# Optimization experiments

Measured on AMD Instinct MI355X. Metric: run time of the kernel, lower is better.

The kernel has to match this reference:

```python
import jax, jax.numpy as jnp
import numpy as np

B, T, NINP, NHID = 64, 256, 256, 512
NTOK0, NTOK1 = 2048, 512


def _lstm_cell(x, h, c, Wih, bih, Whh, bhh):
    # PyTorch LSTMCell gate order: i, f, g, o
    g = x @ Wih.T + bih + h @ Whh.T + bhh
    i, f, gg, o = jnp.split(g, 4, axis=-1)
    c_new = jax.nn.sigmoid(f) * c + jax.nn.sigmoid(i) * jnp.tanh(gg)
    h_new = jax.nn.sigmoid(o) * jnp.tanh(c_new)
    return h_new, c_new


def setup_inputs() -> dict:
    key = jax.random.key(0)
    ks = jax.random.split(key, 16)
    ir = 0.1  # initrange from init_weights
    d = {
        "input0": jax.random.randint(ks[0], (B, T), 0, NTOK0),
        "input1": jax.random.randint(ks[1], (B, T), 0, NTOK1),
        "h_low0": jnp.zeros((B, NHID), jnp.float32),
        "c_low0": jnp.zeros((B, NHID), jnp.float32),
        "h_high0": jnp.zeros((B, NHID), jnp.float32),
        "c_high0": jnp.zeros((B, NHID), jnp.float32),
        "measure_token_idx": 5,
        "emb0": jax.random.uniform(ks[2], (NTOK0, NINP), jnp.float32, -ir, ir),
        "emb1": jax.random.uniform(ks[3], (NTOK1, NINP), jnp.float32, -ir, ir),
        # low cell: input size = ninp*2 + nhid = 1024
        "Wih_low": jax.random.normal(ks[4], (4 * NHID, 2 * NINP + NHID), jnp.float32) * 0.02,
        "bih_low": jnp.zeros((4 * NHID,), jnp.float32),
        "Whh_low": jax.random.normal(ks[5], (4 * NHID, NHID), jnp.float32) * 0.02,
        "bhh_low": jnp.zeros((4 * NHID,), jnp.float32),
        # high cell: input size = nhid
        "Wih_high": jax.random.normal(ks[6], (4 * NHID, NHID), jnp.float32) * 0.02,
        "bih_high": jnp.zeros((4 * NHID,), jnp.float32),
        "Whh_high": jax.random.normal(ks[7], (4 * NHID, NHID), jnp.float32) * 0.02,
        "bhh_high": jnp.zeros((4 * NHID,), jnp.float32),
        "Wdec0": jax.random.uniform(ks[8], (NTOK0, NHID), jnp.float32, -ir, ir),
        "bdec0": jnp.zeros((NTOK0,), jnp.float32),
        "Wdec1": jax.random.uniform(ks[9], (NTOK1, NHID), jnp.float32, -ir, ir),
        "bdec1": jnp.zeros((NTOK1,), jnp.float32),
    }
    return d


def reference(input0, input1, h_low0, c_low0, h_high0, c_high0, measure_token_idx,
              emb0, emb1, Wih_low, bih_low, Whh_low, bhh_low,
              Wih_high, bih_high, Whh_high, bhh_high,
              Wdec0, bdec0, Wdec1, bdec1):
    # Embedding lookups for both channels, concatenated (dropout = identity in eval)
    embs = jnp.concatenate([emb0[input0], emb1[input1]], axis=-1)  # [B,T,2*ninp]
    xs = jnp.swapaxes(embs, 0, 1)                                   # [T,B,2*ninp]
    mask = (input0 == measure_token_idx).astype(embs.dtype)[..., None]  # [B,T,1]
    ms = jnp.swapaxes(mask, 0, 1)                                   # [T,B,1]

    def step(carry, xm):
        h_l, c_l, h_h, c_h = carry
        x_t, m_t = xm
        inp = jnp.concatenate([x_t, h_h], axis=-1)  # [B, 2*ninp+nhid]
        h_l, c_l = _lstm_cell(inp, h_l, c_l, Wih_low, bih_low, Whh_low, bhh_low)
        h_tmp, c_tmp = _lstm_cell(h_l, h_h, c_h, Wih_high, bih_high, Whh_high, bhh_high)
        h_h = m_t * h_tmp + (1.0 - m_t) * h_h  # gated state update at measure boundaries
        c_h = m_t * c_tmp + (1.0 - m_t) * c_h
        return (h_l, c_l, h_h, c_h), h_l

    (h_l, c_l, h_h, c_h), outs = jax.lax.scan(step, (h_low0, c_low0, h_high0, c_high0), (xs, ms))
    output = jnp.swapaxes(outs, 0, 1)  # [B,T,nhid]
    dec0 = output @ Wdec0.T + bdec0    # [B,T,ntok0]
    dec1 = output @ Wdec1.T + bdec1    # [B,T,ntok1]
    return dec0, dec1, h_l, c_l, h_h, c_h
```

## Files before the change

### kernel.cpp

```cpp
#include <hip/hip_runtime.h>
#include <hip/hip_bf16.h>

#define T_ 256
#define B_ 64
#define NWG 32

typedef __attribute__((ext_vector_type(8))) short bf16x8;
typedef __attribute__((ext_vector_type(4))) float f32x4;
typedef __attribute__((ext_vector_type(4))) unsigned uint4v;
union v128 { uint4v u4; bf16x8 h8; };

__device__ __forceinline__ float bf2f(unsigned short u){
  unsigned int i = ((unsigned int)u) << 16;
  float f; __builtin_memcpy(&f, &i, 4); return f;
}
__device__ __forceinline__ unsigned short f2bf(float f){
  __hip_bfloat16 h = __float2bfloat16(f);
  unsigned short u; __builtin_memcpy(&u, &h, 2); return u;
}
__device__ __forceinline__ float fsigm(float x){ return 1.0f/(1.0f + __expf(-x)); }
__device__ __forceinline__ float ftanh(float x){ return 1.0f - 2.0f/(__expf(2.0f*x) + 1.0f); }

__device__ __forceinline__ void ld16_cc_issue(v128* dst, const unsigned short* p){
  asm volatile("global_load_dwordx4 %0, %1, off sc0 sc1" : "=v"(dst->u4) : "v"(p) : "memory");
}
__device__ __forceinline__ void st8_cc(unsigned short* p, unsigned long long v){
  asm volatile("global_store_dwordx2 %0, %1, off sc0 sc1" :: "v"(p), "v"(v) : "memory");
}
__device__ __forceinline__ unsigned long long ld8_cc(const unsigned short* p){
  unsigned long long v;
  asm volatile("global_load_dwordx2 %0, %1, off sc0 sc1\n\ts_waitcnt vmcnt(0)"
               : "=v"(v) : "v"(p) : "memory");
  return v;
}

__global__ void k_prep(const int* __restrict__ in0, const int* __restrict__ in1,
                       const int* __restrict__ mtok,
                       const float* __restrict__ emb0, const float* __restrict__ emb1,
                       const float* __restrict__ Wih_low, const float* __restrict__ Whh_low_f,
                       const float* __restrict__ Wih_high_f, const float* __restrict__ Whh_high_f,
                       const float* __restrict__ Wdec0_f, const float* __restrict__ Wdec1_f,
                       unsigned short* __restrict__ W0, unsigned short* __restrict__ Wlh,
                       unsigned short* __restrict__ Whhl, unsigned short* __restrict__ Wihh,
                       unsigned short* __restrict__ Whhh, unsigned short* __restrict__ Wd0,
                       unsigned short* __restrict__ Wd1, unsigned short* __restrict__ E,
                       float* __restrict__ mask, unsigned* __restrict__ stepflag,
                       unsigned* __restrict__ bar)
{
  int gid = blockIdx.x*blockDim.x + threadIdx.x;
  int gsz = gridDim.x*blockDim.x;
  for (int i=gid; i<2048*512; i+=gsz){
    int r = i>>9, c = i&511;
    W0[i]   = f2bf(Wih_low[(size_t)r*1024 + c]);
    Wlh[i]  = f2bf(Wih_low[(size_t)r*1024 + 512 + c]);
    Whhl[i] = f2bf(Whh_low_f[i]);
    Wihh[i] = f2bf(Wih_high_f[i]);
    Whhh[i] = f2bf(Whh_high_f[i]);
    Wd0[i]  = f2bf(Wdec0_f[i]);
  }
  for (int i=gid; i<512*512; i+=gsz) Wd1[i] = f2bf(Wdec1_f[i]);
  int mt = mtok[0];
  for (int i=gid; i<T_*B_*512; i+=gsz){
    int m = i>>9, k = i&511;
    int t = m>>6, b = m&63;
    float v;
    if (k < 256) v = emb0[(size_t)in0[b*T_+t]*256 + k];
    else         v = emb1[(size_t)in1[b*T_+t]*256 + (k-256)];
    E[i] = f2bf(v);
  }
  for (int i=gid; i<T_*B_; i+=gsz){
    int t = i>>6, b = i&63;
    mask[i] = (in0[b*T_+t] == mt) ? 1.0f : 0.0f;
  }
  for (int i=gid; i<T_; i+=gsz){
    unsigned f = 0;
    for (int b=0;b<B_;b++) f |= (in0[b*T_+i] == mt) ? 1u : 0u;
    stepflag[i] = f;
  }
  for (int i=gid; i<1024; i+=gsz) bar[i] = 0;
}

__launch_bounds__(256)
__global__ void k_gemm(const unsigned short* __restrict__ A,
                       const unsigned short* __restrict__ W,
                       const float* __restrict__ bias1, const float* __restrict__ bias2,
                       unsigned short* __restrict__ out16, float* __restrict__ out32,
                       int N, int mode)
{
  __shared__ unsigned short As[128*40];
  __shared__ unsigned short Bs[128*40];
  const int tid = threadIdx.x;
  const int m0 = blockIdx.x*128, n0 = blockIdx.y*128;
  const int wid = tid>>6, lane = tid&63;
  const int wm = (wid>>1)*64, wn = (wid&1)*64;
  const int lr = lane&15, lk = lane>>4;
  f32x4 acc[4][4] = {};
  for (int k0=0; k0<512; k0+=32){
    __syncthreads();
    #pragma unroll
    for (int i=0;i<2;i++){
      int eb = tid + 256*i;
      int row = eb>>2, kb = eb&3;
      *(bf16x8*)&As[row*40 + kb*8] = *(const bf16x8*)&A[(size_t)(m0+row)*512 + k0 + kb*8];
      *(bf16x8*)&Bs[row*40 + kb*8] = *(const bf16x8*)&W[(size_t)(n0+row)*512 + k0 + kb*8];
    }
    __syncthreads();
    bf16x8 af[4], bff[4];
    #pragma unroll
    for (int i=0;i<4;i++){
      af[i]  = *(const bf16x8*)&As[(wm + i*16 + lr)*40 + lk*8];
      bff[i] = *(const bf16x8*)&Bs[(wn + i*16 + lr)*40 + lk*8];
    }
    #pragma unroll
    for (int mi=0;mi<4;mi++)
      #pragma unroll
      for (int ni=0;ni<4;ni++)
        acc[mi][ni] = __builtin_amdgcn_mfma_f32_16x16x32_bf16(af[mi], bff[ni], acc[mi][ni], 0,0,0);
  }
  #pragma unroll
  for (int mi=0;mi<4;mi++){
    #pragma unroll
    for (int ni=0;ni<4;ni++){
      int n = n0 + wn + ni*16 + lr;
      float bb = bias1 ? bias1[n] : 0.0f;
      if (bias2) bb += bias2[n];
      #pragma unroll
      for (int r=0;r<4;r++){
        int m = m0 + wm + mi*16 + lk*4 + r;
        float v = acc[mi][ni][r] + bb;
        if (mode == 0){
          out16[(size_t)m*N + n] = f2bf(v);
        } else {
          int t = m>>6, b = m&63;
          out32[((size_t)b*T_ + t)*N + n] = v;
        }
      }
    }
  }
}

__device__ __forceinline__ void g_arrive(unsigned* flags, int j, unsigned gen){
  asm volatile("s_waitcnt vmcnt(0)" ::: "memory");
  __syncthreads();
  if (threadIdx.x == 0)
    __hip_atomic_store(&flags[j*32], gen+1u, __ATOMIC_RELAXED, __HIP_MEMORY_SCOPE_AGENT);
  __builtin_amdgcn_sched_barrier(0);
}
__device__ __forceinline__ void g_wait(const unsigned* flags, unsigned gen){
  if (threadIdx.x < 64){
    const unsigned* fp = &flags[(threadIdx.x & (NWG-1))*32];
    for(;;){
      unsigned v = __hip_atomic_load(fp, __ATOMIC_RELAXED, __HIP_MEMORY_SCOPE_AGENT);
      if (__ballot(v >= gen+1u) == ~0ull) break;
      __builtin_amdgcn_s_sleep(1);
    }
  }
  __builtin_amdgcn_sched_barrier(0);
  __syncthreads();
  __builtin_amdgcn_sched_barrier(0);
}

__device__ __forceinline__ void compute_hht(const unsigned short* __restrict__ hh,
                                            const unsigned short* __restrict__ Wlh,
                                            float* hht, int d0, int mb, int lr, int lk)
{
  v128 av[16];
  #pragma unroll
  for (int ks=0;ks<16;ks++)
    ld16_cc_issue(&av[ks], hh + (mb+lr)*512 + ks*32 + lk*8);
  asm volatile("s_waitcnt vmcnt(0)" ::: "memory");
  __builtin_amdgcn_sched_barrier(0);
  f32x4 a[4] = {};
  #pragma unroll
  for (int ks=0;ks<16;ks++){
    #pragma unroll
    for (int g=0; g<4; g++){
      bf16x8 bg = *(const bf16x8*)&Wlh[(size_t)(g*512 + d0 + lr)*512 + ks*32 + lk*8];
      a[g] = __builtin_amdgcn_mfma_f32_16x16x32_bf16(av[ks].h8, bg, a[g], 0,0,0);
    }
  }
  #pragma unroll
  for (int g=0; g<4; g++)
    #pragma unroll
    for (int r=0;r<4;r++){
      int b = mb + lk*4 + r;
      hht[b*68 + g*16 + lr] = a[g][r];
    }
}

__launch_bounds__(256)
__global__ void k_recur(const float* __restrict__ h_low0, const float* __restrict__ c_low0,
                        const float* __restrict__ h_high0, const float* __restrict__ c_high0,
                        const float* __restrict__ bih_high, const float* __restrict__ bhh_high,
                        const unsigned short* __restrict__ xW,
                        const unsigned short* __restrict__ Whhl,
                        const unsigned short* __restrict__ Wlh,
                        const unsigned short* __restrict__ Wihh,
                        const unsigned short* __restrict__ Whhh,
                        const float* __restrict__ mask, const unsigned* __restrict__ stepflag,
                        unsigned short* __restrict__ hl_buf, unsigned short* __restrict__ hh_buf,
                        unsigned short* __restrict__ hseq, unsigned* bar,
                        float* __restrict__ outS)
{
  __shared__ unsigned short Ws[64*520];
  __shared__ float hht[64*68];
  __shared__ float gb[64*68];
  __shared__ float cl[64*16];
  __shared__ float ch[64*16];
  const int tid = threadIdx.x;
  const int j = blockIdx.x;
  const int d0 = j*16;
  const int wid = tid>>6, lane = tid&63;
  const int lr = lane&15, lk = lane>>4;
  const int mb = wid*16;
  const int eb = tid>>2;
  const int ep = (tid&3)*4;

  for (int i=tid; i<64*64; i+=256){
    int n = i>>6, cb = i&63;
    int grow = (n>>4)*512 + d0 + (n&15);
    *(bf16x8*)&Ws[n*520 + cb*8] = *(const bf16x8*)&Whhl[(size_t)grow*512 + cb*8];
  }
  for (int i=tid; i<1024; i+=256){
    int b=i>>4, dd=i&15;
    cl[i] = c_low0[b*512 + d0 + dd];
    ch[i] = c_high0[b*512 + d0 + dd];
  }
  {
    int gi = eb*512 + d0 + ep;
    unsigned long long l0 = (unsigned long long)f2bf(h_low0[gi])        | ((unsigned long long)f2bf(h_low0[gi+1])<<16)
                          | ((unsigned long long)f2bf(h_low0[gi+2])<<32)| ((unsigned long long)f2bf(h_low0[gi+3])<<48);
    unsigned long long h0 = (unsigned long long)f2bf(h_high0[gi])        | ((unsigned long long)f2bf(h_high0[gi+1])<<16)
                          | ((unsigned long long)f2bf(h_high0[gi+2])<<32)| ((unsigned long long)f2bf(h_high0[gi+3])<<48);
    st8_cc(&hl_buf[gi], l0);
    st8_cc(&hh_buf[gi], h0);
  }
  unsigned gen = 0;
  g_arrive(bar, j, gen);
  g_wait(bar, gen); gen++;
  unsigned long long cxi, cxf, cxg, cxo, nxi, nxf, nxg, nxo;
  {
    size_t xr = (size_t)eb*2048 + d0 + ep;
    cxi = *(const unsigned long long*)&xW[xr];
    cxf = *(const unsigned long long*)&xW[xr + 512];
    cxg = *(const unsigned long long*)&xW[xr + 1024];
    cxo = *(const unsigned long long*)&xW[xr + 1536];
  }
  compute_hht(hh_buf, Wlh, hht, d0, mb, lr, lk);
  __syncthreads();

  int hs = 0;
  for (int t=0; t<T_; t++){
    const int rl = t&1, wl = rl^1;
    const unsigned short* hlr = hl_buf + rl*32768;
    v128 av[16];
    #pragma unroll
    for (int ks=0;ks<16;ks++)
      ld16_cc_issue(&av[ks], hlr + (mb+lr)*512 + ks*32 + lk*8);
    asm volatile("s_waitcnt vmcnt(0)" ::: "memory");
    __builtin_amdgcn_sched_barrier(0);
    if (t+1 < T_){
      size_t xr = ((size_t)(t+1)*64 + eb)*2048 + d0 + ep;
      nxi = *(const unsigned long long*)&xW[xr];
      nxf = *(const unsigned long long*)&xW[xr + 512];
      nxg = *(const unsigned long long*)&xW[xr + 1024];
      nxo = *(const unsigned long long*)&xW[xr + 1536];
    }
    f32x4 a[4] = {};
    #pragma unroll
    for (int ks=0;ks<16;ks++){
      #pragma unroll
      for (int g=0; g<4; g++){
        bf16x8 bg = *(const bf16x8*)&Ws[(g*16+lr)*520 + ks*32 + lk*8];
        a[g] = __builtin_amdgcn_mfma_f32_16x16x32_bf16(av[ks].h8, bg, a[g], 0,0,0);
      }
    }
    #pragma unroll
    for (int g=0; g<4; g++)
      #pragma unroll
      for (int r=0;r<4;r++){
        int b = mb + lk*4 + r;
        gb[b*68 + g*16 + lr] = a[g][r] + hht[b*68 + g*16 + lr];
      }
    unsigned long long hp;
    {
      const int b = eb;
      unsigned short hb[4];
      #pragma unroll
      for (int q=0;q<4;q++){
        int dd = ep + q;
        float g_i = gb[b*68 + dd]      + bf2f((unsigned short)(cxi >> (16*q)));
        float g_f = gb[b*68 + 16 + dd] + bf2f((unsigned short)(cxf >> (16*q)));
        float g_g = gb[b*68 + 32 + dd] + bf2f((unsigned short)(cxg >> (16*q)));
        float g_o = gb[b*68 + 48 + dd] + bf2f((unsigned short)(cxo >> (16*q)));
        float c = fsigm(g_f)*cl[b*16+dd] + fsigm(g_i)*ftanh(g_g);
        float h = fsigm(g_o)*ftanh(c);
        cl[b*16+dd] = c;
        hb[q] = f2bf(h);
      }
      hp = (unsigned long long)hb[0] | ((unsigned long long)hb[1]<<16)
         | ((unsigned long long)hb[2]<<32) | ((unsigned long long)hb[3]<<48);
      st8_cc(&hl_buf[wl*32768 + b*512 + d0 + ep], hp);
      *(unsigned long long*)&hseq[((size_t)t*64 + b)*512 + d0 + ep] = hp;
    }
    g_arrive(bar, j, gen);
    g_wait(bar, gen); gen++;
    cxi = nxi; cxf = nxf; cxg = nxg; cxo = nxo;
    if (stepflag[t]){
      const unsigned short* hln = hl_buf + wl*32768;
      const unsigned short* hhr = hh_buf + hs*32768;
      v128 avl[16], avh[16];
      #pragma unroll
      for (int ks=0;ks<16;ks++){
        ld16_cc_issue(&avl[ks], hln + (mb+lr)*512 + ks*32 + lk*8);
        ld16_cc_issue(&avh[ks], hhr + (mb+lr)*512 + ks*32 + lk*8);
      }
      asm volatile("s_waitcnt vmcnt(0)" ::: "memory");
      __builtin_amdgcn_sched_barrier(0);
      f32x4 hacc[4] = {};
      #pragma unroll
      for (int ks=0;ks<16;ks++){
        #pragma unroll
        for (int g=0; g<4; g++){
          size_t grw = (size_t)(g*512 + d0 + lr)*512 + ks*32 + lk*8;
          bf16x8 bi = *(const bf16x8*)&Wihh[grw];
          bf16x8 bh = *(const bf16x8*)&Whhh[grw];
          hacc[g] = __builtin_amdgcn_mfma_f32_16x16x32_bf16(avl[ks].h8, bi, hacc[g], 0,0,0);
          hacc[g] = __builtin_amdgcn_mfma_f32_16x16x32_bf16(avh[ks].h8, bh, hacc[g], 0,0,0);
        }
      }
      #pragma unroll
      for (int g=0; g<4; g++)
        #pragma unroll
        for (int r=0;r<4;r++){
          int b = mb + lk*4 + r;
          gb[b*68 + g*16 + lr] = hacc[g][r];
        }
      {
        const int b = eb;
        float m = mask[t*64 + b];
        unsigned long long hold4 = ld8_cc(&hh_buf[hs*32768 + b*512 + d0 + ep]);
        unsigned short hn[4];
        #pragma unroll
        for (int q=0;q<4;q++){
          int dd = ep + q; int d = d0 + dd;
          float g_i = gb[b*68+dd]      + bih_high[d]      + bhh_high[d];
          float g_f = gb[b*68+16+dd]   + bih_high[512+d]  + bhh_high[512+d];
          float g_g = gb[b*68+32+dd]   + bih_high[1024+d] + bhh_high[1024+d];
          float g_o = gb[b*68+48+dd]   + bih_high[1536+d] + bhh_high[1536+d];
          float ct = fsigm(g_f)*ch[b*16+dd] + fsigm(g_i)*ftanh(g_g);
          float ht = fsigm(g_o)*ftanh(ct);
          float hold = bf2f((unsigned short)(hold4 >> (16*q)));
          hn[q] = f2bf(m*ht + (1.0f-m)*hold);
          ch[b*16+dd] = m*ct + (1.0f-m)*ch[b*16+dd];
        }
        unsigned long long hq = (unsigned long long)hn[0] | ((unsigned long long)hn[1]<<16)
                              | ((unsigned long long)hn[2]<<32) | ((unsigned long long)hn[3]<<48);
        st8_cc(&hh_buf[(hs^1)*32768 + eb*512 + d0 + ep], hq);
      }
      g_arrive(bar, j, gen);
      g_wait(bar, gen); gen++;
      hs ^= 1;
      compute_hht(hh_buf + hs*32768, Wlh, hht, d0, mb, lr, lk);
      __syncthreads();
    }
  }
  {
    int gi = eb*512 + d0 + ep;
    unsigned long long hl4 = ld8_cc(&hl_buf[gi]);
    unsigned long long hh4 = ld8_cc(&hh_buf[hs*32768 + gi]);
    #pragma unroll
    for (int q=0;q<4;q++){
      outS[gi+q]           = bf2f((unsigned short)(hl4 >> (16*q)));
      outS[32768 + gi + q] = cl[eb*16 + ep + q];
      outS[65536 + gi + q] = bf2f((unsigned short)(hh4 >> (16*q)));
      outS[98304 + gi + q] = ch[eb*16 + ep + q];
    }
  }
}

extern "C" void kernel_launch(void* const* d_in, const int* in_sizes, int n_in,
                              void* d_out, int out_size, void* d_ws, size_t ws_size,
                              hipStream_t stream)
{
  const int*   in0    = (const int*)  d_in[0];
  const int*   in1    = (const int*)  d_in[1];
  const float* hl0    = (const float*)d_in[2];
  const float* cl0    = (const float*)d_in[3];
  const float* hh0    = (const float*)d_in[4];
  const float* ch0    = (const float*)d_in[5];
  const int*   mtok   = (const int*)  d_in[6];
  const float* emb0   = (const float*)d_in[7];
  const float* emb1   = (const float*)d_in[8];
  const float* Wihl_f = (const float*)d_in[9];
  const float* bihl   = (const float*)d_in[10];
  const float* Whhl_f = (const float*)d_in[11];
  const float* bhhl   = (const float*)d_in[12];
  const float* Wihh_f = (const float*)d_in[13];
  const float* bihh   = (const float*)d_in[14];
  const float* Whhh_f = (const float*)d_in[15];
  const float* bhhh   = (const float*)d_in[16];
  const float* Wd0_f  = (const float*)d_in[17];
  const float* bd0    = (const float*)d_in[18];
  const float* Wd1_f  = (const float*)d_in[19];
  const float* bd1    = (const float*)d_in[20];

  float* dout = (float*)d_out;
  unsigned short* xW = (unsigned short*)dout;
  unsigned short* E  = (unsigned short*)(dout + 33554432);

  char* ws = (char*)d_ws;
  unsigned short* hseq = (unsigned short*)(ws + 0);
  unsigned short* W0   = (unsigned short*)(ws + 16777216);
  unsigned short* Wlh  = (unsigned short*)(ws + 18874368);
  unsigned short* Whhl = (unsigned short*)(ws + 20971520);
  unsigned short* Wihh = (unsigned short*)(ws + 23068672);
  unsigned short* Whhh = (unsigned short*)(ws + 25165824);
  unsigned short* Wd0  = (unsigned short*)(ws + 27262976);
  unsigned short* Wd1  = (unsigned short*)(ws + 29360128);
  unsigned short* hlb  = (unsigned short*)(ws + 29884416);
  unsigned short* hhb  = (unsigned short*)(ws + 30015488);
  float*          mask = (float*)    (ws + 30146560);
  unsigned*       sflg = (unsigned*) (ws + 30212096);
  unsigned*       bar  = (unsigned*) (ws + 30213120);

  k_prep<<<2048, 256, 0, stream>>>(in0,in1,mtok,emb0,emb1,Wihl_f,Whhl_f,Wihh_f,Whhh_f,Wd0_f,Wd1_f,
                                   W0,Wlh,Whhl,Wihh,Whhh,Wd0,Wd1,E,mask,sflg,bar);
  dim3 g1(128,16);
  k_gemm<<<g1, 256, 0, stream>>>(E, W0, bihl, bhhl, xW, nullptr, 2048, 0);
  k_recur<<<NWG, 256, 0, stream>>>(hl0,cl0,hh0,ch0,bihh,bhhh,xW,Whhl,Wlh,Wihh,Whhh,
                                   mask,sflg,hlb,hhb,hseq,bar,dout + 41943040);
  k_gemm<<<g1, 256, 0, stream>>>(hseq, Wd0, bd0, nullptr, nullptr, dout, 2048, 1);
  dim3 g2(128,4);
  k_gemm<<<g2, 256, 0, stream>>>(hseq, Wd1, bd1, nullptr, nullptr, dout + 33554432, 512, 1);
}
```

Measured before the change: 1.941 ms.

## Replace per-step grid barrier with generation-tagged data blocks polled directly

The per-timestep global barrier across the 32 recurrent workgroups is removed. Each hidden-state chunk is instead stored as a 16-byte block carrying a generation counter, and consumers poll until every block they need holds the expected generation. The high-cell update likewise uses tagged blocks, and its Wih/Whh MFMA passes are split so the low-state half can start before the high-state data arrives. This removes barrier round-trips from the sequential critical path. The cost is double-sized state buffers, extra polling traffic, and reliance on 16-byte stores becoming visible atomically.

```diff
diff --git a/kernel.cpp b/kernel.cpp
--- a/kernel.cpp
+++ b/kernel.cpp
@@ -21,17 +21,49 @@
 __device__ __forceinline__ float fsigm(float x){ return 1.0f/(1.0f + __expf(-x)); }
 __device__ __forceinline__ float ftanh(float x){ return 1.0f - 2.0f/(__expf(2.0f*x) + 1.0f); }
 
-__device__ __forceinline__ void ld16_cc_issue(v128* dst, const unsigned short* p){
-  asm volatile("global_load_dwordx4 %0, %1, off sc0 sc1" : "=v"(dst->u4) : "v"(p) : "memory");
-}
-__device__ __forceinline__ void st8_cc(unsigned short* p, unsigned long long v){
-  asm volatile("global_store_dwordx2 %0, %1, off sc0 sc1" :: "v"(p), "v"(v) : "memory");
-}
-__device__ __forceinline__ unsigned long long ld8_cc(const unsigned short* p){
+__device__ __forceinline__ unsigned long long ld8_cc(const void* p){
   unsigned long long v;
   asm volatile("global_load_dwordx2 %0, %1, off sc0 sc1\n\ts_waitcnt vmcnt(0)"
                : "=v"(v) : "v"(p) : "memory");
   return v;
+}
+__device__ __forceinline__ void st_blk(void* base, int p, int b, int kb,
+                                       unsigned d01, unsigned d23, unsigned gen){
+  uint4v v; v[0]=d01; v[1]=d23; v[2]=gen; v[3]=0u;
+  void* addr = (char*)base + ((((size_t)p*64 + b)*128 + kb)<<4);
+  asm volatile("global_store_dwordx4 %0, %1, off sc0 sc1" :: "v"(addr), "v"(v) : "memory");
+}
+
+#define LD4(dst, off) asm volatile("global_load_dwordx4 %0, %1, off offset:" #off " sc0 sc1" \
+                                   : "=v"(dst) : "v"(ab) : "memory")
+
+__device__ __forceinline__ void poll_read(const char* ab, unsigned need, v128 blk[16][2]){
+  for(;;){
+    LD4(blk[0][0].u4, 0);     LD4(blk[0][1].u4, 16);
+    LD4(blk[1][0].u4, 128);   LD4(blk[1][1].u4, 144);
+    LD4(blk[2][0].u4, 256);   LD4(blk[2][1].u4, 272);
+    LD4(blk[3][0].u4, 384);   LD4(blk[3][1].u4, 400);
+    LD4(blk[4][0].u4, 512);   LD4(blk[4][1].u4, 528);
+    LD4(blk[5][0].u4, 640);   LD4(blk[5][1].u4, 656);
+    LD4(blk[6][0].u4, 768);   LD4(blk[6][1].u4, 784);
+    LD4(blk[7][0].u4, 896);   LD4(blk[7][1].u4, 912);
+    LD4(blk[8][0].u4, 1024);  LD4(blk[8][1].u4, 1040);
+    LD4(blk[9][0].u4, 1152);  LD4(blk[9][1].u4, 1168);
+    LD4(blk[10][0].u4, 1280); LD4(blk[10][1].u4, 1296);
+    LD4(blk[11][0].u4, 1408); LD4(blk[11][1].u4, 1424);
+    LD4(blk[12][0].u4, 1536); LD4(blk[12][1].u4, 1552);
+    LD4(blk[13][0].u4, 1664); LD4(blk[13][1].u4, 1680);
+    LD4(blk[14][0].u4, 1792); LD4(blk[14][1].u4, 1808);
+    LD4(blk[15][0].u4, 1920); LD4(blk[15][1].u4, 1936);
+    asm volatile("s_waitcnt vmcnt(0)" ::: "memory");
+    bool ok = true;
+    #pragma unroll
+    for (int ks=0;ks<16;ks++)
+      ok = ok && (blk[ks][0].u4[2] >= need) && (blk[ks][1].u4[2] >= need);
+    if (__ballot(ok) == ~0ull) break;
+    __builtin_amdgcn_s_sleep(1);
+  }
+  __builtin_amdgcn_sched_barrier(0);
 }
 
 __global__ void k_prep(const int* __restrict__ in0, const int* __restrict__ in1,
@@ -45,7 +77,8 @@
                        unsigned short* __restrict__ Whhh, unsigned short* __restrict__ Wd0,
                        unsigned short* __restrict__ Wd1, unsigned short* __restrict__ E,
                        float* __restrict__ mask, unsigned* __restrict__ stepflag,
-                       unsigned* __restrict__ bar)
+                       unsigned* __restrict__ bar,
+                       uint4v* __restrict__ hlP, uint4v* __restrict__ hhP)
 {
   int gid = blockIdx.x*blockDim.x + threadIdx.x;
   int gsz = gridDim.x*blockDim.x;
@@ -78,6 +111,8 @@
     stepflag[i] = f;
   }
   for (int i=gid; i<1024; i+=gsz) bar[i] = 0;
+  uint4v z; z[0]=0u; z[1]=0u; z[2]=0u; z[3]=0u;
+  for (int i=gid; i<2*64*128; i+=gsz){ hlP[i] = z; hhP[i] = z; }
 }
 
 __launch_bounds__(256)
@@ -139,53 +174,25 @@
   }
 }
 
-__device__ __forceinline__ void g_arrive(unsigned* flags, int j, unsigned gen){
+__device__ __forceinline__ void g_arrive(unsigned* flags, int j){
   asm volatile("s_waitcnt vmcnt(0)" ::: "memory");
   __syncthreads();
   if (threadIdx.x == 0)
-    __hip_atomic_store(&flags[j*32], gen+1u, __ATOMIC_RELAXED, __HIP_MEMORY_SCOPE_AGENT);
+    __hip_atomic_store(&flags[j*32], 1u, __ATOMIC_RELAXED, __HIP_MEMORY_SCOPE_AGENT);
   __builtin_amdgcn_sched_barrier(0);
 }
-__device__ __forceinline__ void g_wait(const unsigned* flags, unsigned gen){
+__device__ __forceinline__ void g_wait(const unsigned* flags){
   if (threadIdx.x < 64){
     const unsigned* fp = &flags[(threadIdx.x & (NWG-1))*32];
     for(;;){
       unsigned v = __hip_atomic_load(fp, __ATOMIC_RELAXED, __HIP_MEMORY_SCOPE_AGENT);
-      if (__ballot(v >= gen+1u) == ~0ull) break;
+      if (__ballot(v >= 1u) == ~0ull) break;
       __builtin_amdgcn_s_sleep(1);
     }
   }
   __builtin_amdgcn_sched_barrier(0);
   __syncthreads();
   __builtin_amdgcn_sched_barrier(0);
-}
-
-__device__ __forceinline__ void compute_hht(const unsigned short* __restrict__ hh,
-                                            const unsigned short* __restrict__ Wlh,
-                                            float* hht, int d0, int mb, int lr, int lk)
-{
-  v128 av[16];
-  #pragma unroll
-  for (int ks=0;ks<16;ks++)
-    ld16_cc_issue(&av[ks], hh + (mb+lr)*512 + ks*32 + lk*8);
-  asm volatile("s_waitcnt vmcnt(0)" ::: "memory");
-  __builtin_amdgcn_sched_barrier(0);
-  f32x4 a[4] = {};
-  #pragma unroll
-  for (int ks=0;ks<16;ks++){
-    #pragma unroll
-    for (int g=0; g<4; g++){
-      bf16x8 bg = *(const bf16x8*)&Wlh[(size_t)(g*512 + d0 + lr)*512 + ks*32 + lk*8];
-      a[g] = __builtin_amdgcn_mfma_f32_16x16x32_bf16(av[ks].h8, bg, a[g], 0,0,0);
-    }
-  }
-  #pragma unroll
-  for (int g=0; g<4; g++)
-    #pragma unroll
-    for (int r=0;r<4;r++){
-      int b = mb + lk*4 + r;
-      hht[b*68 + g*16 + lr] = a[g][r];
-    }
 }
 
 __launch_bounds__(256)
@@ -198,7 +205,7 @@
                         const unsigned short* __restrict__ Wihh,
                         const unsigned short* __restrict__ Whhh,
                         const float* __restrict__ mask, const unsigned* __restrict__ stepflag,
-                        unsigned short* __restrict__ hl_buf, unsigned short* __restrict__ hh_buf,
+                        char* __restrict__ hlP, char* __restrict__ hhP,
                         unsigned short* __restrict__ hseq, unsigned* bar,
                         float* __restrict__ outS)
 {
@@ -214,7 +221,9 @@
   const int lr = lane&15, lk = lane>>4;
   const int mb = wid*16;
   const int eb = tid>>2;
-  const int ep = (tid&3)*4;
+  const int eq = tid&3;
+  const int ep = eq*4;
+  const int kb = j*4 + eq;
 
   for (int i=tid; i<64*64; i+=256){
     int n = i>>6, cb = i&63;
@@ -228,16 +237,19 @@
   }
   {
     int gi = eb*512 + d0 + ep;
-    unsigned long long l0 = (unsigned long long)f2bf(h_low0[gi])        | ((unsigned long long)f2bf(h_low0[gi+1])<<16)
-                          | ((unsigned long long)f2bf(h_low0[gi+2])<<32)| ((unsigned long long)f2bf(h_low0[gi+3])<<48);
-    unsigned long long h0 = (unsigned long long)f2bf(h_high0[gi])        | ((unsigned long long)f2bf(h_high0[gi+1])<<16)
-                          | ((unsigned long long)f2bf(h_high0[gi+2])<<32)| ((unsigned long long)f2bf(h_high0[gi+3])<<48);
-    st8_cc(&hl_buf[gi], l0);
-    st8_cc(&hh_buf[gi], h0);
-  }
-  unsigned gen = 0;
-  g_arrive(bar, j, gen);
-  g_wait(bar, gen); gen++;
+    unsigned l01 = (unsigned)f2bf(h_low0[gi])   | ((unsigned)f2bf(h_low0[gi+1])<<16);
+    unsigned l23 = (unsigned)f2bf(h_low0[gi+2]) | ((unsigned)f2bf(h_low0[gi+3])<<16);
+    unsigned h01 = (unsigned)f2bf(h_high0[gi])  | ((unsigned)f2bf(h_high0[gi+1])<<16);
+    unsigned h23 = (unsigned)f2bf(h_high0[gi+2])| ((unsigned)f2bf(h_high0[gi+3])<<16);
+    st_blk(hlP, 0, eb, kb, l01, l23, 0u);
+    st_blk(hhP, 0, eb, kb, h01, h23, 0u);
+  }
+  g_arrive(bar, j);
+  g_wait(bar);
+
+  const size_t rowoff = ((size_t)(mb+lr)*128 + lk*2) << 4;
+  const size_t paroff = (size_t)64*128*16;
+
   unsigned long long cxi, cxf, cxg, cxo, nxi, nxf, nxg, nxo;
   {
     size_t xr = (size_t)eb*2048 + d0 + ep;
@@ -246,19 +258,31 @@
     cxg = *(const unsigned long long*)&xW[xr + 1024];
     cxo = *(const unsigned long long*)&xW[xr + 1536];
   }
-  compute_hht(hh_buf, Wlh, hht, d0, mb, lr, lk);
-  __syncthreads();
+  v128 blk[16][2];
+  {
+    poll_read(hhP + rowoff, 0u, blk);
+    f32x4 a[4] = {};
+    #pragma unroll
+    for (int ks=0;ks<16;ks++){
+      v128 u; u.u4[0]=blk[ks][0].u4[0]; u.u4[1]=blk[ks][0].u4[1];
+              u.u4[2]=blk[ks][1].u4[0]; u.u4[3]=blk[ks][1].u4[1];
+      #pragma unroll
+      for (int g=0; g<4; g++){
+        bf16x8 bg = *(const bf16x8*)&Wlh[(size_t)(g*512 + d0 + lr)*512 + ks*32 + lk*8];
+        a[g] = __builtin_amdgcn_mfma_f32_16x16x32_bf16(u.h8, bg, a[g], 0,0,0);
+      }
+    }
+    #pragma unroll
+    for (int g=0; g<4; g++)
+      #pragma unroll
+      for (int r=0;r<4;r++) hht[(mb + lk*4 + r)*68 + g*16 + lr] = a[g][r];
+  }
 
   int hs = 0;
+  unsigned hhneed = 0;
   for (int t=0; t<T_; t++){
     const int rl = t&1, wl = rl^1;
-    const unsigned short* hlr = hl_buf + rl*32768;
-    v128 av[16];
-    #pragma unroll
-    for (int ks=0;ks<16;ks++)
-      ld16_cc_issue(&av[ks], hlr + (mb+lr)*512 + ks*32 + lk*8);
-    asm volatile("s_waitcnt vmcnt(0)" ::: "memory");
-    __builtin_amdgcn_sched_barrier(0);
+    poll_read(hlP + (size_t)rl*paroff + rowoff, (unsigned)t, blk);
     if (t+1 < T_){
       size_t xr = ((size_t)(t+1)*64 + eb)*2048 + d0 + ep;
       nxi = *(const unsigned long long*)&xW[xr];
@@ -269,10 +293,12 @@
     f32x4 a[4] = {};
     #pragma unroll
     for (int ks=0;ks<16;ks++){
+      v128 u; u.u4[0]=blk[ks][0].u4[0]; u.u4[1]=blk[ks][0].u4[1];
+              u.u4[2]=blk[ks][1].u4[0]; u.u4[3]=blk[ks][1].u4[1];
       #pragma unroll
       for (int g=0; g<4; g++){
         bf16x8 bg = *(const bf16x8*)&Ws[(g*16+lr)*520 + ks*32 + lk*8];
-        a[g] = __builtin_amdgcn_mfma_f32_16x16x32_bf16(av[ks].h8, bg, a[g], 0,0,0);
+        a[g] = __builtin_amdgcn_mfma_f32_16x16x32_bf16(u.h8, bg, a[g], 0,0,0);
       }
     }
     #pragma unroll
@@ -282,7 +308,6 @@
         int b = mb + lk*4 + r;
         gb[b*68 + g*16 + lr] = a[g][r] + hht[b*68 + g*16 + lr];
       }
-    unsigned long long hp;
     {
       const int b = eb;
       unsigned short hb[4];
@@ -298,35 +323,35 @@
         cl[b*16+dd] = c;
         hb[q] = f2bf(h);
       }
-      hp = (unsigned long long)hb[0] | ((unsigned long long)hb[1]<<16)
-         | ((unsigned long long)hb[2]<<32) | ((unsigned long long)hb[3]<<48);
-      st8_cc(&hl_buf[wl*32768 + b*512 + d0 + ep], hp);
-      *(unsigned long long*)&hseq[((size_t)t*64 + b)*512 + d0 + ep] = hp;
-    }
-    g_arrive(bar, j, gen);
-    g_wait(bar, gen); gen++;
+      unsigned d01 = (unsigned)hb[0] | ((unsigned)hb[1]<<16);
+      unsigned d23 = (unsigned)hb[2] | ((unsigned)hb[3]<<16);
+      st_blk(hlP, wl, b, kb, d01, d23, (unsigned)(t+1));
+      *(unsigned long long*)&hseq[((size_t)t*64 + b)*512 + d0 + ep] =
+          (unsigned long long)d01 | ((unsigned long long)d23<<32);
+    }
     cxi = nxi; cxf = nxf; cxg = nxg; cxo = nxo;
     if (stepflag[t]){
-      const unsigned short* hln = hl_buf + wl*32768;
-      const unsigned short* hhr = hh_buf + hs*32768;
-      v128 avl[16], avh[16];
+      f32x4 hacc[4] = {};
+      poll_read(hlP + (size_t)wl*paroff + rowoff, (unsigned)(t+1), blk);
       #pragma unroll
       for (int ks=0;ks<16;ks++){
-        ld16_cc_issue(&avl[ks], hln + (mb+lr)*512 + ks*32 + lk*8);
-        ld16_cc_issue(&avh[ks], hhr + (mb+lr)*512 + ks*32 + lk*8);
-      }
-      asm volatile("s_waitcnt vmcnt(0)" ::: "memory");
-      __builtin_amdgcn_sched_barrier(0);
-      f32x4 hacc[4] = {};
+        v128 u; u.u4[0]=blk[ks][0].u4[0]; u.u4[1]=blk[ks][0].u4[1];
+                u.u4[2]=blk[ks][1].u4[0]; u.u4[3]=blk[ks][1].u4[1];
+        #pragma unroll
+        for (int g=0; g<4; g++){
+          bf16x8 bi = *(const bf16x8*)&Wihh[(size_t)(g*512 + d0 + lr)*512 + ks*32 + lk*8];
+          hacc[g] = __builtin_amdgcn_mfma_f32_16x16x32_bf16(u.h8, bi, hacc[g], 0,0,0);
+        }
+      }
+      poll_read(hhP + (size_t)hs*paroff + rowoff, hhneed, blk);
       #pragma unroll
       for (int ks=0;ks<16;ks++){
+        v128 u; u.u4[0]=blk[ks][0].u4[0]; u.u4[1]=blk[ks][0].u4[1];
+                u.u4[2]=blk[ks][1].u4[0]; u.u4[3]=blk[ks][1].u4[1];
         #pragma unroll
         for (int g=0; g<4; g++){
-          size_t grw = (size_t)(g*512 + d0 + lr)*512 + ks*32 + lk*8;
-          bf16x8 bi = *(const bf16x8*)&Wihh[grw];
-          bf16x8 bh = *(const bf16x8*)&Whhh[grw];
-          hacc[g] = __builtin_amdgcn_mfma_f32_16x16x32_bf16(avl[ks].h8, bi, hacc[g], 0,0,0);
-          hacc[g] = __builtin_amdgcn_mfma_f32_16x16x32_bf16(avh[ks].h8, bh, hacc[g], 0,0,0);
+          bf16x8 bh = *(const bf16x8*)&Whhh[(size_t)(g*512 + d0 + lr)*512 + ks*32 + lk*8];
+          hacc[g] = __builtin_amdgcn_mfma_f32_16x16x32_bf16(u.h8, bh, hacc[g], 0,0,0);
         }
       }
       #pragma unroll
@@ -339,7 +364,7 @@
       {
         const int b = eb;
         float m = mask[t*64 + b];
-        unsigned long long hold4 = ld8_cc(&hh_buf[hs*32768 + b*512 + d0 + ep]);
+        unsigned long long hold4 = ld8_cc(hhP + (size_t)hs*paroff + ((((size_t)b)*128 + kb)<<4));
         unsigned short hn[4];
         #pragma unroll
         for (int q=0;q<4;q++){
@@ -354,21 +379,36 @@
           hn[q] = f2bf(m*ht + (1.0f-m)*hold);
           ch[b*16+dd] = m*ct + (1.0f-m)*ch[b*16+dd];
         }
-        unsigned long long hq = (unsigned long long)hn[0] | ((unsigned long long)hn[1]<<16)
-                              | ((unsigned long long)hn[2]<<32) | ((unsigned long long)hn[3]<<48);
-        st8_cc(&hh_buf[(hs^1)*32768 + eb*512 + d0 + ep], hq);
-      }
-      g_arrive(bar, j, gen);
-      g_wait(bar, gen); gen++;
+        unsigned d01 = (unsigned)hn[0] | ((unsigned)hn[1]<<16);
+        unsigned d23 = (unsigned)hn[2] | ((unsigned)hn[3]<<16);
+        st_blk(hhP, hs^1, b, kb, d01, d23, hhneed + 1u);
+      }
+      poll_read(hhP + (size_t)(hs^1)*paroff + rowoff, hhneed + 1u, blk);
+      {
+        f32x4 a2[4] = {};
+        #pragma unroll
+        for (int ks=0;ks<16;ks++){
+          v128 u; u.u4[0]=blk[ks][0].u4[0]; u.u4[1]=blk[ks][0].u4[1];
+                  u.u4[2]=blk[ks][1].u4[0]; u.u4[3]=blk[ks][1].u4[1];
+          #pragma unroll
+          for (int g=0; g<4; g++){
+            bf16x8 bg = *(const bf16x8*)&Wlh[(size_t)(g*512 + d0 + lr)*512 + ks*32 + lk*8];
+            a2[g] = __builtin_amdgcn_mfma_f32_16x16x32_bf16(u.h8, bg, a2[g], 0,0,0);
+          }
+        }
+        #pragma unroll
+        for (int g=0; g<4; g++)
+          #pragma unroll
+          for (int r=0;r<4;r++) hht[(mb + lk*4 + r)*68 + g*16 + lr] = a2[g][r];
+      }
       hs ^= 1;
-      compute_hht(hh_buf + hs*32768, Wlh, hht, d0, mb, lr, lk);
-      __syncthreads();
+      hhneed += 1u;
     }
   }
   {
     int gi = eb*512 + d0 + ep;
-    unsigned long long hl4 = ld8_cc(&hl_buf[gi]);
-    unsigned long long hh4 = ld8_cc(&hh_buf[hs*32768 + gi]);
+    unsigned long long hl4 = ld8_cc(hlP + ((((size_t)eb)*128 + kb)<<4));
+    unsigned long long hh4 = ld8_cc(hhP + (size_t)hs*paroff + ((((size_t)eb)*128 + kb)<<4));
     #pragma unroll
     for (int q=0;q<4;q++){
       outS[gi+q]           = bf2f((unsigned short)(hl4 >> (16*q)));
@@ -418,18 +458,19 @@
   unsigned short* Whhh = (unsigned short*)(ws + 25165824);
   unsigned short* Wd0  = (unsigned short*)(ws + 27262976);
   unsigned short* Wd1  = (unsigned short*)(ws + 29360128);
-  unsigned short* hlb  = (unsigned short*)(ws + 29884416);
-  unsigned short* hhb  = (unsigned short*)(ws + 30015488);
-  float*          mask = (float*)    (ws + 30146560);
-  unsigned*       sflg = (unsigned*) (ws + 30212096);
-  unsigned*       bar  = (unsigned*) (ws + 30213120);
+  char*           hlP  = ws + 29884416;
+  char*           hhP  = ws + 30146560;
+  float*          mask = (float*)    (ws + 30408704);
+  unsigned*       sflg = (unsigned*) (ws + 30474240);
+  unsigned*       bar  = (unsigned*) (ws + 30475264);
 
   k_prep<<<2048, 256, 0, stream>>>(in0,in1,mtok,emb0,emb1,Wihl_f,Whhl_f,Wihh_f,Whhh_f,Wd0_f,Wd1_f,
-                                   W0,Wlh,Whhl,Wihh,Whhh,Wd0,Wd1,E,mask,sflg,bar);
+                                   W0,Wlh,Whhl,Wihh,Whhh,Wd0,Wd1,E,mask,sflg,bar,
+                                   (uint4v*)hlP,(uint4v*)hhP);
   dim3 g1(128,16);
   k_gemm<<<g1, 256, 0, stream>>>(E, W0, bihl, bhhl, xW, nullptr, 2048, 0);
   k_recur<<<NWG, 256, 0, stream>>>(hl0,cl0,hh0,ch0,bihh,bhhh,xW,Whhl,Wlh,Wihh,Whhh,
-                                   mask,sflg,hlb,hhb,hseq,bar,dout + 41943040);
+                                   mask,sflg,hlP,hhP,hseq,bar,dout + 41943040);
   k_gemm<<<g1, 256, 0, stream>>>(hseq, Wd0, bd0, nullptr, nullptr, dout, 2048, 1);
   dim3 g2(128,4);
   k_gemm<<<g2, 256, 0, stream>>>(hseq, Wd1, bd1, nullptr, nullptr, dout + 33554432, 512, 1);
```

After: 3.617 ms. 86.3% more time.
